# Optimization experiments

Measured on AMD Instinct MI355X. Metric: run time of the kernel, lower is better.

Reference implementation:

```python
import jax, jax.numpy as jnp
import numpy as np

HIDDEN = 1024
HEADS = 16
HEAD_DIM = HIDDEN // HEADS


def setup_inputs() -> dict:
    key = jax.random.key(0)
    k1, k2, k3, k4, k5 = jax.random.split(key, 5)
    B, S = 2, 2048
    x = jax.random.normal(k1, (B, S, HIDDEN), dtype=jnp.float32)
    attention_mask = jnp.ones((B, S), dtype=jnp.int32)
    scale = 1.0 / np.sqrt(HIDDEN)
    W_qkv = jax.random.normal(k2, (HIDDEN, 3 * HIDDEN), dtype=jnp.float32) * scale
    b_qkv = jnp.zeros((3 * HIDDEN,), dtype=jnp.float32)
    W_out = jax.random.normal(k3, (HIDDEN, HIDDEN), dtype=jnp.float32) * scale
    b_out = jnp.zeros((HIDDEN,), dtype=jnp.float32)
    return {"x": x, "attention_mask": attention_mask, "W_qkv": W_qkv,
            "b_qkv": b_qkv, "W_out": W_out, "b_out": b_out}


def reference(x, attention_mask, W_qkv, b_qkv, W_out, b_out):
    B, S, H = x.shape
    qkv = x @ W_qkv + b_qkv                       # [B,S,3H]
    q, k, v = jnp.split(qkv, 3, axis=-1)
    def heads(t):
        return t.reshape(B, S, HEADS, HEAD_DIM).transpose(0, 2, 1, 3)  # [B,h,S,d]
    q, k, v = heads(q), heads(k), heads(v)
    scale = 1.0 / np.sqrt(HEAD_DIM).astype(np.float32)
    scores = jnp.einsum('bhsd,bhtd->bhst', q, k) * scale  # [B,h,S,S]
    causal = jnp.triu(jnp.full((S, S), -jnp.inf, dtype=scores.dtype), k=1)
    scores = scores + causal
    pad = (attention_mask == 0)[:, None, None, :]          # [B,1,1,S]
    scores = jnp.where(pad, -jnp.inf, scores)
    probs = jax.nn.softmax(scores, axis=-1)
    context = jnp.einsum('bhst,bhtd->bhsd', probs, v)
    context = context.transpose(0, 2, 1, 3).reshape(B, S, H)
    output = context @ W_out + b_out
    return (output, q, k, v)
```

## Files before the change

kernel.cpp:

```cpp
#include <hip/hip_runtime.h>
#include <hip/hip_bf16.h>
#include <stdint.h>

typedef __attribute__((ext_vector_type(8))) short bf16x8;
typedef __attribute__((ext_vector_type(4))) float f32x4;

#define GLD16(gp, lp) __builtin_amdgcn_global_load_lds( \
    (const __attribute__((address_space(1))) void*)(gp), \
    (__attribute__((address_space(3))) void*)(lp), 16, 0, 0)

struct bf16_4 { __hip_bfloat16 x, y, z, w; };

__global__ __launch_bounds__(256) void k_conv(const float* __restrict__ in,
                                              __hip_bfloat16* __restrict__ out, int n4)
{
    int i = blockIdx.x * 256 + threadIdx.x;
    if (i >= n4) return;
    float4 v = ((const float4*)in)[i];
    bf16_4 o = { __float2bfloat16(v.x), __float2bfloat16(v.y),
                 __float2bfloat16(v.z), __float2bfloat16(v.w) };
    ((bf16_4*)out)[i] = o;
}

__global__ __launch_bounds__(256) void k_tconv(const float* __restrict__ in,
                                               __hip_bfloat16* __restrict__ out,
                                               int R, int C)
{
    __shared__ float tile[32][33];
    int c0 = blockIdx.x * 32, r0 = blockIdx.y * 32;
    int tc = threadIdx.x & 31, tr = threadIdx.x >> 5;
#pragma unroll
    for (int i = 0; i < 4; i++)
        tile[tr + i * 8][tc] = in[(size_t)(r0 + tr + i * 8) * C + c0 + tc];
    __syncthreads();
#pragma unroll
    for (int i = 0; i < 4; i++) {
        int r = tr + i * 8;
        out[(size_t)(c0 + r) * R + r0 + tc] = __float2bfloat16(tile[tc][r]);
    }
}

__global__ __launch_bounds__(256) void k_vtrans(const __hip_bfloat16* __restrict__ vin,
                                                __hip_bfloat16* __restrict__ vout)
{
    __shared__ __hip_bfloat16 t[64 * 80];
    const int kt = blockIdx.x, bh = blockIdx.y;
    const int tid = threadIdx.x;
    const size_t ib = (size_t)bh * 131072;
#pragma unroll
    for (int i = 0; i < 2; i++) {
        int c = i * 256 + tid;
        int kv = c >> 3, d0 = (c & 7) * 8;
        bf16x8 vv = *(const bf16x8*)(vin + ib + (size_t)(kt * 64 + kv) * 64 + d0);
#pragma unroll
        for (int j = 0; j < 8; j++)
            t[(d0 + j) * 80 + kv] = ((const __hip_bfloat16*)&vv)[j];
    }
    __syncthreads();
#pragma unroll
    for (int i = 0; i < 2; i++) {
        int c = i * 256 + tid;
        int d = c >> 3, kv0 = (c & 7) * 8;
        *(bf16x8*)(vout + ib + (size_t)d * 2048 + kt * 64 + kv0) =
            *(const bf16x8*)(t + d * 80 + kv0);
    }
}

template <int BM, int BN, int TM, int TN, int EPI>
__global__ __launch_bounds__(TM * TN * 64, 2) void k_gemm2(
    const __hip_bfloat16* __restrict__ A,
    const __hip_bfloat16* __restrict__ Bt,
    const float* __restrict__ bias,
    float* __restrict__ outf,
    __hip_bfloat16* __restrict__ outb,
    int M, int N, int K)
{
    constexpr int THREADS = TM * TN * 64;
    constexpr int NMI = BM / TM / 16;
    constexpr int NNI = BN / TN / 16;
    constexpr int ACH = BM * 8 / THREADS;
    constexpr int BCH = BN * 8 / THREADS;

    __shared__ __hip_bfloat16 As[2][BM * 64];
    __shared__ __hip_bfloat16 Bs[2][BN * 64];

    const int tid  = threadIdx.x;
    const int lane = tid & 63, wid = tid >> 6;
    const int wm = wid / TN, wn = wid % TN;
    const int lr = lane & 15, lg = lane >> 4;
    const int m0 = blockIdx.y * BM, n0 = blockIdx.x * BN;
    const int NT = K >> 6;

    f32x4 acc[NMI][NNI] = {};

    auto stage = [&](int bb, int t) {
#pragma unroll
        for (int i = 0; i < ACH; i++) {
            int c = i * THREADS + tid;
            int r = c >> 3, sl = c & 7;
            GLD16(A + (size_t)(m0 + r) * K + t * 64 + ((sl ^ (r & 7)) * 8),
                  &As[bb][(size_t)(i * THREADS + wid * 64) * 8]);
        }
#pragma unroll
        for (int i = 0; i < BCH; i++) {
            int c = i * THREADS + tid;
            int r = c >> 3, sl = c & 7;
            GLD16(Bt + (size_t)(n0 + r) * K + t * 64 + ((sl ^ (r & 7)) * 8),
                  &Bs[bb][(size_t)(i * THREADS + wid * 64) * 8]);
        }
    };

    stage(0, 0);
    __syncthreads();
    int cur = 0;
#pragma unroll 1
    for (int t = 0; t < NT; ++t) {
        if (t + 1 < NT) stage(cur ^ 1, t + 1);
        __builtin_amdgcn_s_setprio(1);
        bf16x8 bfr[NNI][2];
#pragma unroll
        for (int ni = 0; ni < NNI; ni++) {
            int r = wn * (BN / TN) + ni * 16 + lr;
#pragma unroll
            for (int kk = 0; kk < 2; kk++)
                bfr[ni][kk] = *(const bf16x8*)(&Bs[cur][r * 64 + (((kk * 4 + lg) ^ (r & 7)) * 8)]);
        }
#pragma unroll
        for (int mi = 0; mi < NMI; mi++) {
            int r = wm * (BM / TM) + mi * 16 + lr;
            bf16x8 a0 = *(const bf16x8*)(&As[cur][r * 64 + (((0 + lg) ^ (r & 7)) * 8)]);
            bf16x8 a1 = *(const bf16x8*)(&As[cur][r * 64 + (((4 + lg) ^ (r & 7)) * 8)]);
#pragma unroll
            for (int ni = 0; ni < NNI; ni++) {
                acc[mi][ni] = __builtin_amdgcn_mfma_f32_16x16x32_bf16(a0, bfr[ni][0], acc[mi][ni], 0, 0, 0);
                acc[mi][ni] = __builtin_amdgcn_mfma_f32_16x16x32_bf16(a1, bfr[ni][1], acc[mi][ni], 0, 0, 0);
            }
        }
        __builtin_amdgcn_s_setprio(0);
        __syncthreads();
        cur ^= 1;
    }

#pragma unroll
    for (int mi = 0; mi < NMI; mi++) {
#pragma unroll
        for (int ni = 0; ni < NNI; ni++) {
#pragma unroll
            for (int j = 0; j < 4; j++) {
                int mg = m0 + wm * (BM / TM) + mi * 16 + 4 * lg + j;
                int ng = n0 + wn * (BN / TN) + ni * 16 + lr;
                float val = acc[mi][ni][j] + bias[ng];
                if (EPI == 0) {
                    int part = ng >> 10;
                    int h    = (ng >> 6) & 15;
                    int dd   = ng & 63;
                    int b    = mg >> 11;
                    int s    = mg & 2047;
                    size_t idx = ((size_t)part << 22) + ((((size_t)b * 16 + h) * 2048 + s) << 6) + dd;
                    outf[idx] = val;
                    outb[idx] = __float2bfloat16(val);
                } else {
                    outf[(size_t)mg * N + ng] = val;
                }
            }
        }
    }
}

__global__ __launch_bounds__(256, 3) void k_attn2(const __hip_bfloat16* __restrict__ qkv,
                                                  const __hip_bfloat16* __restrict__ vT,
                                                  const int* __restrict__ amask,
                                                  __hip_bfloat16* __restrict__ ctx)
{
    const int bx = blockIdx.x;
    const int bh = blockIdx.y;
    const int b = bh >> 4, h = bh & 15;
    const int tid = threadIdx.x;
    const int lane = tid & 63, w = tid >> 6;
    const int lr = lane & 15, lg = lane >> 4;
    const size_t hb = (size_t)bh * (2048 * 64);
    const __hip_bfloat16* qg = qkv + hb;
    const __hip_bfloat16* kg = qkv + ((size_t)1 << 22) + hb;
    const __hip_bfloat16* vt = vT + (size_t)bh * (64 * 2048);

    __shared__ __hip_bfloat16 Ks[128 * 64];
    __shared__ __hip_bfloat16 Vs[64 * 128];
    __shared__ __hip_bfloat16 Ps[4][16 * 128];
    __shared__ float maskadd[128];

#pragma unroll 1
    for (int pass = 0; pass < 2; ++pass) {
        const int qt = pass ? bx : (31 - bx);
        const int q0 = qt * 64;
        const int nkt = (64 * qt + 191) >> 7;

        bf16x8 qf[2];
#pragma unroll
        for (int kk = 0; kk < 2; kk++)
            qf[kk] = *(const bf16x8*)(qg + (size_t)(q0 + w * 16 + lr) * 64 + kk * 32 + 8 * lg);

        f32x4 of[4] = {};
        float m_run[4], l_run[4];
#pragma unroll
        for (int j = 0; j < 4; j++) { m_run[j] = -1e30f; l_run[j] = 0.f; }
        const int rowg = q0 + w * 16 + 4 * lg;

#pragma unroll 1
        for (int kt = 0; kt < nkt; ++kt) {
            const int k0 = kt * 128;
            __syncthreads();
#pragma unroll
            for (int i = 0; i < 4; i++) {
                int c = i * 256 + tid;
                int r = c >> 3, sl = c & 7;
                GLD16(kg + (size_t)(k0 + r) * 64 + ((sl ^ (r & 7)) * 8),
                      Ks + (size_t)(i * 256 + w * 64) * 8);
            }
#pragma unroll
            for (int i = 0; i < 4; i++) {
                int c = i * 256 + tid;
                int r = c >> 4, sl = c & 15;
                GLD16(vt + (size_t)r * 2048 + k0 + ((sl ^ (r & 15)) * 8),
                      Vs + (size_t)(i * 256 + w * 64) * 8);
            }
            if (tid < 128) maskadd[tid] = amask[b * 2048 + k0 + tid] ? 0.f : -1e30f;
            __syncthreads();

            f32x4 sa[8] = {};
#pragma unroll
            for (int ni = 0; ni < 8; ni++) {
                int r = ni * 16 + lr;
#pragma unroll
                for (int kk = 0; kk < 2; kk++) {
                    bf16x8 kf = *(const bf16x8*)(Ks + (size_t)r * 64 + (((kk * 4 + lg) ^ (r & 7)) * 8));
                    sa[ni] = __builtin_amdgcn_mfma_f32_16x16x32_bf16(qf[kk], kf, sa[ni], 0, 0, 0);
                }
            }
#pragma unroll
            for (int ni = 0; ni < 8; ni++) {
                int colg = k0 + ni * 16 + lr;
                float ma = maskadd[ni * 16 + lr];
#pragma unroll
                for (int j = 0; j < 4; j++) {
                    float val = sa[ni][j] * 0.125f + ma;
                    if (colg > rowg + j) val = -1e30f;
                    sa[ni][j] = val;
                }
            }
            float mnew[4], corr[4];
#pragma unroll
            for (int j = 0; j < 4; j++) {
                float t = fmaxf(fmaxf(fmaxf(sa[0][j], sa[1][j]), fmaxf(sa[2][j], sa[3][j])),
                                fmaxf(fmaxf(sa[4][j], sa[5][j]), fmaxf(sa[6][j], sa[7][j])));
                t = fmaxf(t, __shfl_xor(t, 1));
                t = fmaxf(t, __shfl_xor(t, 2));
                t = fmaxf(t, __shfl_xor(t, 4));
                t = fmaxf(t, __shfl_xor(t, 8));
                mnew[j] = fmaxf(m_run[j], t);
                corr[j] = __expf(m_run[j] - mnew[j]);
                m_run[j] = mnew[j];
            }
            float tsum[4] = {0.f, 0.f, 0.f, 0.f};
#pragma unroll
            for (int ni = 0; ni < 8; ni++)
#pragma unroll
                for (int j = 0; j < 4; j++) {
                    float p = __expf(sa[ni][j] - mnew[j]);
                    sa[ni][j] = p;
                    tsum[j] += p;
                }
#pragma unroll
            for (int j = 0; j < 4; j++) {
                float t = tsum[j];
                t += __shfl_xor(t, 1);
                t += __shfl_xor(t, 2);
                t += __shfl_xor(t, 4);
                t += __shfl_xor(t, 8);
                l_run[j] = l_run[j] * corr[j] + t;
#pragma unroll
                for (int nd = 0; nd < 4; nd++) of[nd][j] *= corr[j];
            }
#pragma unroll
            for (int ni = 0; ni < 8; ni++)
#pragma unroll
                for (int j = 0; j < 4; j++) {
                    int row = 4 * lg + j, col = ni * 16 + lr;
                    Ps[w][row * 128 + (((col >> 3) ^ row) * 8) + (col & 7)] =
                        __float2bfloat16(sa[ni][j]);
                }
            asm volatile("s_waitcnt lgkmcnt(0)" ::: "memory");
            __builtin_amdgcn_sched_barrier(0);
#pragma unroll
            for (int kk = 0; kk < 4; kk++) {
                bf16x8 pf = *(const bf16x8*)(&Ps[w][lr * 128 + (((kk * 4 + lg) ^ lr) * 8)]);
#pragma unroll
                for (int nd = 0; nd < 4; nd++) {
                    int r = nd * 16 + lr;
                    bf16x8 vf = *(const bf16x8*)(Vs + (size_t)r * 128 + (((kk * 4 + lg) ^ (r & 15)) * 8));
                    of[nd] = __builtin_amdgcn_mfma_f32_16x16x32_bf16(pf, vf, of[nd], 0, 0, 0);
                }
            }
        }
#pragma unroll
        for (int j = 0; j < 4; j++) {
            float inv = 1.f / l_run[j];
            int s = rowg + j;
            size_t base = ((size_t)b * 2048 + s) * 1024 + h * 64;
#pragma unroll
            for (int nd = 0; nd < 4; nd++)
                ctx[base + nd * 16 + lr] = __float2bfloat16(of[nd][j] * inv);
        }
    }
}

extern "C" void kernel_launch(void* const* d_in, const int* in_sizes, int n_in,
                              void* d_out, int out_size, void* d_ws, size_t ws_size,
                              hipStream_t stream)
{
    const float* x    = (const float*)d_in[0];
    const int*   am   = (const int*)d_in[1];
    const float* Wqkv = (const float*)d_in[2];
    const float* bqkv = (const float*)d_in[3];
    const float* Wout = (const float*)d_in[4];
    const float* bout = (const float*)d_in[5];
    float* out = (float*)d_out;

    char* ws = (char*)d_ws;
    __hip_bfloat16* x_bf   = (__hip_bfloat16*)(ws);
    __hip_bfloat16* Wqkv_t = (__hip_bfloat16*)(ws + ((size_t)8 << 20));
    __hip_bfloat16* Wout_t = (__hip_bfloat16*)(ws + ((size_t)14 << 20));
    __hip_bfloat16* qkv_bf = (__hip_bfloat16*)(ws + ((size_t)16 << 20));
    __hip_bfloat16* ctx_bf = (__hip_bfloat16*)(ws + ((size_t)40 << 20));
    __hip_bfloat16* vT     = x_bf;

    k_conv<<<4096, 256, 0, stream>>>(x, x_bf, 1048576);
    k_tconv<<<dim3(96, 32), 256, 0, stream>>>(Wqkv, Wqkv_t, 1024, 3072);
    k_tconv<<<dim3(32, 32), 256, 0, stream>>>(Wout, Wout_t, 1024, 1024);
    k_gemm2<256, 192, 2, 4, 0><<<dim3(16, 16), 512, 0, stream>>>(
        x_bf, Wqkv_t, bqkv, out + ((size_t)1 << 22), qkv_bf, 4096, 3072, 1024);
    k_vtrans<<<dim3(32, 32), 256, 0, stream>>>(qkv_bf + ((size_t)2 << 22), vT);
    k_attn2<<<dim3(16, 32), 256, 0, stream>>>(qkv_bf, vT, am, ctx_bf);
    k_gemm2<128, 128, 2, 2, 1><<<dim3(8, 32), 256, 0, stream>>>(
        ctx_bf, Wout_t, bout, out, nullptr, 4096, 1024, 1024);
}
```

Before: 231.6 us.

## Restructure attention to read K/V from global memory, one Q tile per block

The attention kernel stops staging K and V tiles in shared memory and loads MFMA operands directly from global memory (through L2/L1), which removes the block-wide barriers. The two-pass causal load pairing is replaced by one query tile per block on a 32x32 grid with a higher occupancy hint. The mask is loaded per lane, and the causal masking branch is skipped for tiles entirely below the diagonal. Softmax switches to exp2 with the scale folded in by log2(e). Direct global loads are uncoalesced and rely on cache hits, and dropping the pass pairing gives up the causal load balancing.

```diff
diff --git a/kernel.cpp b/kernel.cpp
--- a/kernel.cpp
+++ b/kernel.cpp
@@ -1,6 +1,7 @@
 #include <hip/hip_runtime.h>
 #include <hip/hip_bf16.h>
 #include <stdint.h>
+#include <math.h>
 
 typedef __attribute__((ext_vector_type(8))) short bf16x8;
 typedef __attribute__((ext_vector_type(4))) float f32x4;
@@ -167,149 +168,134 @@
     }
 }
 
-__global__ __launch_bounds__(256, 3) void k_attn2(const __hip_bfloat16* __restrict__ qkv,
+__global__ __launch_bounds__(256, 4) void k_attn3(const __hip_bfloat16* __restrict__ qkv,
                                                   const __hip_bfloat16* __restrict__ vT,
                                                   const int* __restrict__ amask,
                                                   __hip_bfloat16* __restrict__ ctx)
 {
-    const int bx = blockIdx.x;
+    const int qt = 31 - blockIdx.x;
     const int bh = blockIdx.y;
     const int b = bh >> 4, h = bh & 15;
     const int tid = threadIdx.x;
     const int lane = tid & 63, w = tid >> 6;
     const int lr = lane & 15, lg = lane >> 4;
+    const int q0 = qt * 64;
     const size_t hb = (size_t)bh * (2048 * 64);
     const __hip_bfloat16* qg = qkv + hb;
     const __hip_bfloat16* kg = qkv + ((size_t)1 << 22) + hb;
     const __hip_bfloat16* vt = vT + (size_t)bh * (64 * 2048);
 
-    __shared__ __hip_bfloat16 Ks[128 * 64];
-    __shared__ __hip_bfloat16 Vs[64 * 128];
     __shared__ __hip_bfloat16 Ps[4][16 * 128];
-    __shared__ float maskadd[128];
+
+    bf16x8 qf[2];
+#pragma unroll
+    for (int kk = 0; kk < 2; kk++)
+        qf[kk] = *(const bf16x8*)(qg + (size_t)(q0 + w * 16 + lr) * 64 + kk * 32 + 8 * lg);
+
+    f32x4 of[4] = {};
+    float m_run[4], l_run[4];
+#pragma unroll
+    for (int j = 0; j < 4; j++) { m_run[j] = -1e30f; l_run[j] = 0.f; }
+    const int wrow0 = q0 + w * 16;
+    const int rowg = wrow0 + 4 * lg;
+    const int nkt = (q0 + 64 + 127) >> 7;
+    const float SC = 0.18033688011112042f;
 
 #pragma unroll 1
-    for (int pass = 0; pass < 2; ++pass) {
-        const int qt = pass ? bx : (31 - bx);
-        const int q0 = qt * 64;
-        const int nkt = (64 * qt + 191) >> 7;
-
-        bf16x8 qf[2];
-#pragma unroll
-        for (int kk = 0; kk < 2; kk++)
-            qf[kk] = *(const bf16x8*)(qg + (size_t)(q0 + w * 16 + lr) * 64 + kk * 32 + 8 * lg);
-
-        f32x4 of[4] = {};
-        float m_run[4], l_run[4];
-#pragma unroll
-        for (int j = 0; j < 4; j++) { m_run[j] = -1e30f; l_run[j] = 0.f; }
-        const int rowg = q0 + w * 16 + 4 * lg;
-
-#pragma unroll 1
-        for (int kt = 0; kt < nkt; ++kt) {
-            const int k0 = kt * 128;
-            __syncthreads();
-#pragma unroll
-            for (int i = 0; i < 4; i++) {
-                int c = i * 256 + tid;
-                int r = c >> 3, sl = c & 7;
-                GLD16(kg + (size_t)(k0 + r) * 64 + ((sl ^ (r & 7)) * 8),
-                      Ks + (size_t)(i * 256 + w * 64) * 8);
-            }
-#pragma unroll
-            for (int i = 0; i < 4; i++) {
-                int c = i * 256 + tid;
-                int r = c >> 4, sl = c & 15;
-                GLD16(vt + (size_t)r * 2048 + k0 + ((sl ^ (r & 15)) * 8),
-                      Vs + (size_t)(i * 256 + w * 64) * 8);
-            }
-            if (tid < 128) maskadd[tid] = amask[b * 2048 + k0 + tid] ? 0.f : -1e30f;
-            __syncthreads();
-
-            f32x4 sa[8] = {};
-#pragma unroll
-            for (int ni = 0; ni < 8; ni++) {
-                int r = ni * 16 + lr;
-#pragma unroll
-                for (int kk = 0; kk < 2; kk++) {
-                    bf16x8 kf = *(const bf16x8*)(Ks + (size_t)r * 64 + (((kk * 4 + lg) ^ (r & 7)) * 8));
-                    sa[ni] = __builtin_amdgcn_mfma_f32_16x16x32_bf16(qf[kk], kf, sa[ni], 0, 0, 0);
-                }
-            }
+    for (int kt = 0; kt < nkt; ++kt) {
+        const int k0 = kt * 128;
+        float ma[8];
+#pragma unroll
+        for (int ni = 0; ni < 8; ni++)
+            ma[ni] = amask[b * 2048 + k0 + ni * 16 + lr] ? 0.f : -1e30f;
+        f32x4 sa[8] = {};
+#pragma unroll
+        for (int ni = 0; ni < 8; ni++) {
+#pragma unroll
+            for (int kk = 0; kk < 2; kk++) {
+                bf16x8 kf = *(const bf16x8*)(kg + (size_t)(k0 + ni * 16 + lr) * 64 + kk * 32 + 8 * lg);
+                sa[ni] = __builtin_amdgcn_mfma_f32_16x16x32_bf16(qf[kk], kf, sa[ni], 0, 0, 0);
+            }
+        }
+        if (k0 + 127 <= wrow0) {
+#pragma unroll
+            for (int ni = 0; ni < 8; ni++)
+#pragma unroll
+                for (int j = 0; j < 4; j++)
+                    sa[ni][j] = fmaf(sa[ni][j], SC, ma[ni]);
+        } else {
 #pragma unroll
             for (int ni = 0; ni < 8; ni++) {
                 int colg = k0 + ni * 16 + lr;
-                float ma = maskadd[ni * 16 + lr];
 #pragma unroll
                 for (int j = 0; j < 4; j++) {
-                    float val = sa[ni][j] * 0.125f + ma;
+                    float val = fmaf(sa[ni][j], SC, ma[ni]);
                     if (colg > rowg + j) val = -1e30f;
                     sa[ni][j] = val;
                 }
             }
-            float mnew[4], corr[4];
+        }
+        float mnew[4], corr[4];
+#pragma unroll
+        for (int j = 0; j < 4; j++) {
+            float t = fmaxf(fmaxf(fmaxf(sa[0][j], sa[1][j]), fmaxf(sa[2][j], sa[3][j])),
+                            fmaxf(fmaxf(sa[4][j], sa[5][j]), fmaxf(sa[6][j], sa[7][j])));
+            t = fmaxf(t, __shfl_xor(t, 1));
+            t = fmaxf(t, __shfl_xor(t, 2));
+            t = fmaxf(t, __shfl_xor(t, 4));
+            t = fmaxf(t, __shfl_xor(t, 8));
+            mnew[j] = fmaxf(m_run[j], t);
+            corr[j] = exp2f(m_run[j] - mnew[j]);
+            m_run[j] = mnew[j];
+        }
+        float tsum[4] = {0.f, 0.f, 0.f, 0.f};
+#pragma unroll
+        for (int ni = 0; ni < 8; ni++)
 #pragma unroll
             for (int j = 0; j < 4; j++) {
-                float t = fmaxf(fmaxf(fmaxf(sa[0][j], sa[1][j]), fmaxf(sa[2][j], sa[3][j])),
-                                fmaxf(fmaxf(sa[4][j], sa[5][j]), fmaxf(sa[6][j], sa[7][j])));
-                t = fmaxf(t, __shfl_xor(t, 1));
-                t = fmaxf(t, __shfl_xor(t, 2));
-                t = fmaxf(t, __shfl_xor(t, 4));
-                t = fmaxf(t, __shfl_xor(t, 8));
-                mnew[j] = fmaxf(m_run[j], t);
-                corr[j] = __expf(m_run[j] - mnew[j]);
-                m_run[j] = mnew[j];
-            }
-            float tsum[4] = {0.f, 0.f, 0.f, 0.f};
-#pragma unroll
-            for (int ni = 0; ni < 8; ni++)
-#pragma unroll
-                for (int j = 0; j < 4; j++) {
-                    float p = __expf(sa[ni][j] - mnew[j]);
-                    sa[ni][j] = p;
-                    tsum[j] += p;
-                }
+                float p = exp2f(sa[ni][j] - mnew[j]);
+                sa[ni][j] = p;
+                tsum[j] += p;
+            }
+#pragma unroll
+        for (int j = 0; j < 4; j++) {
+            float t = tsum[j];
+            t += __shfl_xor(t, 1);
+            t += __shfl_xor(t, 2);
+            t += __shfl_xor(t, 4);
+            t += __shfl_xor(t, 8);
+            l_run[j] = l_run[j] * corr[j] + t;
+#pragma unroll
+            for (int nd = 0; nd < 4; nd++) of[nd][j] *= corr[j];
+        }
+#pragma unroll
+        for (int ni = 0; ni < 8; ni++)
 #pragma unroll
             for (int j = 0; j < 4; j++) {
-                float t = tsum[j];
-                t += __shfl_xor(t, 1);
-                t += __shfl_xor(t, 2);
-                t += __shfl_xor(t, 4);
-                t += __shfl_xor(t, 8);
-                l_run[j] = l_run[j] * corr[j] + t;
-#pragma unroll
-                for (int nd = 0; nd < 4; nd++) of[nd][j] *= corr[j];
-            }
-#pragma unroll
-            for (int ni = 0; ni < 8; ni++)
-#pragma unroll
-                for (int j = 0; j < 4; j++) {
-                    int row = 4 * lg + j, col = ni * 16 + lr;
-                    Ps[w][row * 128 + (((col >> 3) ^ row) * 8) + (col & 7)] =
-                        __float2bfloat16(sa[ni][j]);
-                }
-            asm volatile("s_waitcnt lgkmcnt(0)" ::: "memory");
-            __builtin_amdgcn_sched_barrier(0);
-#pragma unroll
-            for (int kk = 0; kk < 4; kk++) {
-                bf16x8 pf = *(const bf16x8*)(&Ps[w][lr * 128 + (((kk * 4 + lg) ^ lr) * 8)]);
-#pragma unroll
-                for (int nd = 0; nd < 4; nd++) {
-                    int r = nd * 16 + lr;
-                    bf16x8 vf = *(const bf16x8*)(Vs + (size_t)r * 128 + (((kk * 4 + lg) ^ (r & 15)) * 8));
-                    of[nd] = __builtin_amdgcn_mfma_f32_16x16x32_bf16(pf, vf, of[nd], 0, 0, 0);
-                }
-            }
-        }
-#pragma unroll
-        for (int j = 0; j < 4; j++) {
-            float inv = 1.f / l_run[j];
-            int s = rowg + j;
-            size_t base = ((size_t)b * 2048 + s) * 1024 + h * 64;
-#pragma unroll
-            for (int nd = 0; nd < 4; nd++)
-                ctx[base + nd * 16 + lr] = __float2bfloat16(of[nd][j] * inv);
-        }
+                int row = 4 * lg + j, col = ni * 16 + lr;
+                Ps[w][row * 128 + (((col >> 3) ^ row) * 8) + (col & 7)] =
+                    __float2bfloat16(sa[ni][j]);
+            }
+        asm volatile("s_waitcnt lgkmcnt(0)" ::: "memory");
+        __builtin_amdgcn_sched_barrier(0);
+#pragma unroll
+        for (int kk = 0; kk < 4; kk++) {
+            bf16x8 pf = *(const bf16x8*)(&Ps[w][lr * 128 + (((kk * 4 + lg) ^ lr) * 8)]);
+#pragma unroll
+            for (int nd = 0; nd < 4; nd++) {
+                bf16x8 vf = *(const bf16x8*)(vt + (size_t)(nd * 16 + lr) * 2048 + k0 + kk * 32 + 8 * lg);
+                of[nd] = __builtin_amdgcn_mfma_f32_16x16x32_bf16(pf, vf, of[nd], 0, 0, 0);
+            }
+        }
+    }
+#pragma unroll
+    for (int j = 0; j < 4; j++) {
+        float inv = 1.f / l_run[j];
+        int s = rowg + j;
+        size_t base = ((size_t)b * 2048 + s) * 1024 + h * 64;
+#pragma unroll
+        for (int nd = 0; nd < 4; nd++)
+            ctx[base + nd * 16 + lr] = __float2bfloat16(of[nd][j] * inv);
     }
 }
 
@@ -339,7 +325,7 @@
     k_gemm2<256, 192, 2, 4, 0><<<dim3(16, 16), 512, 0, stream>>>(
         x_bf, Wqkv_t, bqkv, out + ((size_t)1 << 22), qkv_bf, 4096, 3072, 1024);
     k_vtrans<<<dim3(32, 32), 256, 0, stream>>>(qkv_bf + ((size_t)2 << 22), vT);
-    k_attn2<<<dim3(16, 32), 256, 0, stream>>>(qkv_bf, vT, am, ctx_bf);
+    k_attn3<<<dim3(32, 32), 256, 0, stream>>>(qkv_bf, vT, am, ctx_bf);
     k_gemm2<128, 128, 2, 2, 1><<<dim3(8, 32), 256, 0, stream>>>(
         ctx_bf, Wout_t, bout, out, nullptr, 4096, 1024, 1024);
 }
```

New measurement: 534.7 us. 131% more time.

## Register-prefetch next K/V tile in attention, use exp2 softmax and skip mask

Applied to the files above, without the earlier changes.

The attention kernel now loads the next K/V tile into registers while computing the current one, then stores it to LDS at the start of the next iteration. This replaces the direct global-to-LDS loads and is meant to hide global latency. It also folds log2(e) into the score scale so softmax can use exp2f, skips the causal compare on tiles that lie entirely below the diagonal, and raises wave priority around the MFMA blocks. The cost is extra VGPRs for the prefetch buffers, which at launch bounds (256,3) could cause spills or lower occupancy.

```diff
diff --git a/kernel.cpp b/kernel.cpp
--- a/kernel.cpp
+++ b/kernel.cpp
@@ -1,6 +1,7 @@
 #include <hip/hip_runtime.h>
 #include <hip/hip_bf16.h>
 #include <stdint.h>
+#include <math.h>
 
 typedef __attribute__((ext_vector_type(8))) short bf16x8;
 typedef __attribute__((ext_vector_type(4))) float f32x4;
@@ -167,7 +168,7 @@
     }
 }
 
-__global__ __launch_bounds__(256, 3) void k_attn2(const __hip_bfloat16* __restrict__ qkv,
+__global__ __launch_bounds__(256, 3) void k_attn5(const __hip_bfloat16* __restrict__ qkv,
                                                   const __hip_bfloat16* __restrict__ vT,
                                                   const int* __restrict__ amask,
                                                   __hip_bfloat16* __restrict__ ctx)
@@ -188,6 +189,8 @@
     __shared__ __hip_bfloat16 Ps[4][16 * 128];
     __shared__ float maskadd[128];
 
+    const float SC = 0.18033688011112042f;
+
 #pragma unroll 1
     for (int pass = 0; pass < 2; ++pass) {
         const int qt = pass ? bx : (31 - bx);
@@ -203,7 +206,16 @@
         float m_run[4], l_run[4];
 #pragma unroll
         for (int j = 0; j < 4; j++) { m_run[j] = -1e30f; l_run[j] = 0.f; }
-        const int rowg = q0 + w * 16 + 4 * lg;
+        const int wrow0 = q0 + w * 16;
+        const int rowg = wrow0 + 4 * lg;
+
+        bf16x8 kreg[4], vreg[4];
+#pragma unroll
+        for (int i = 0; i < 4; i++) {
+            int c = i * 256 + tid;
+            kreg[i] = *(const bf16x8*)(kg + (size_t)(c >> 3) * 64 + (c & 7) * 8);
+            vreg[i] = *(const bf16x8*)(vt + (size_t)(c >> 4) * 2048 + (c & 15) * 8);
+        }
 
 #pragma unroll 1
         for (int kt = 0; kt < nkt; ++kt) {
@@ -212,20 +224,25 @@
 #pragma unroll
             for (int i = 0; i < 4; i++) {
                 int c = i * 256 + tid;
-                int r = c >> 3, sl = c & 7;
-                GLD16(kg + (size_t)(k0 + r) * 64 + ((sl ^ (r & 7)) * 8),
-                      Ks + (size_t)(i * 256 + w * 64) * 8);
-            }
-#pragma unroll
-            for (int i = 0; i < 4; i++) {
-                int c = i * 256 + tid;
-                int r = c >> 4, sl = c & 15;
-                GLD16(vt + (size_t)r * 2048 + k0 + ((sl ^ (r & 15)) * 8),
-                      Vs + (size_t)(i * 256 + w * 64) * 8);
+                int kr = c >> 3, ksl = c & 7;
+                *(bf16x8*)(Ks + (size_t)kr * 64 + ((ksl ^ (kr & 7)) * 8)) = kreg[i];
+                int vr = c >> 4, vsl = c & 15;
+                *(bf16x8*)(Vs + (size_t)vr * 128 + ((vsl ^ (vr & 15)) * 8)) = vreg[i];
             }
             if (tid < 128) maskadd[tid] = amask[b * 2048 + k0 + tid] ? 0.f : -1e30f;
+            bf16x8 kn[4], vn[4];
+            if (kt + 1 < nkt) {
+                const int k1 = k0 + 128;
+#pragma unroll
+                for (int i = 0; i < 4; i++) {
+                    int c = i * 256 + tid;
+                    kn[i] = *(const bf16x8*)(kg + (size_t)(k1 + (c >> 3)) * 64 + (c & 7) * 8);
+                    vn[i] = *(const bf16x8*)(vt + (size_t)(c >> 4) * 2048 + k1 + (c & 15) * 8);
+                }
+            }
             __syncthreads();
 
+            __builtin_amdgcn_s_setprio(1);
             f32x4 sa[8] = {};
 #pragma unroll
             for (int ni = 0; ni < 8; ni++) {
@@ -236,15 +253,26 @@
                     sa[ni] = __builtin_amdgcn_mfma_f32_16x16x32_bf16(qf[kk], kf, sa[ni], 0, 0, 0);
                 }
             }
-#pragma unroll
-            for (int ni = 0; ni < 8; ni++) {
-                int colg = k0 + ni * 16 + lr;
-                float ma = maskadd[ni * 16 + lr];
-#pragma unroll
-                for (int j = 0; j < 4; j++) {
-                    float val = sa[ni][j] * 0.125f + ma;
-                    if (colg > rowg + j) val = -1e30f;
-                    sa[ni][j] = val;
+            __builtin_amdgcn_s_setprio(0);
+            if (k0 + 127 <= wrow0) {
+#pragma unroll
+                for (int ni = 0; ni < 8; ni++) {
+                    float ma = maskadd[ni * 16 + lr];
+#pragma unroll
+                    for (int j = 0; j < 4; j++)
+                        sa[ni][j] = fmaf(sa[ni][j], SC, ma);
+                }
+            } else {
+#pragma unroll
+                for (int ni = 0; ni < 8; ni++) {
+                    int colg = k0 + ni * 16 + lr;
+                    float ma = maskadd[ni * 16 + lr];
+#pragma unroll
+                    for (int j = 0; j < 4; j++) {
+                        float val = fmaf(sa[ni][j], SC, ma);
+                        if (colg > rowg + j) val = -1e30f;
+                        sa[ni][j] = val;
+                    }
                 }
             }
             float mnew[4], corr[4];
@@ -257,7 +285,7 @@
                 t = fmaxf(t, __shfl_xor(t, 4));
                 t = fmaxf(t, __shfl_xor(t, 8));
                 mnew[j] = fmaxf(m_run[j], t);
-                corr[j] = __expf(m_run[j] - mnew[j]);
+                corr[j] = exp2f(m_run[j] - mnew[j]);
                 m_run[j] = mnew[j];
             }
             float tsum[4] = {0.f, 0.f, 0.f, 0.f};
@@ -265,7 +293,7 @@
             for (int ni = 0; ni < 8; ni++)
 #pragma unroll
                 for (int j = 0; j < 4; j++) {
-                    float p = __expf(sa[ni][j] - mnew[j]);
+                    float p = exp2f(sa[ni][j] - mnew[j]);
                     sa[ni][j] = p;
                     tsum[j] += p;
                 }
@@ -290,6 +318,7 @@
                 }
             asm volatile("s_waitcnt lgkmcnt(0)" ::: "memory");
             __builtin_amdgcn_sched_barrier(0);
+            __builtin_amdgcn_s_setprio(1);
 #pragma unroll
             for (int kk = 0; kk < 4; kk++) {
                 bf16x8 pf = *(const bf16x8*)(&Ps[w][lr * 128 + (((kk * 4 + lg) ^ lr) * 8)]);
@@ -300,6 +329,9 @@
                     of[nd] = __builtin_amdgcn_mfma_f32_16x16x32_bf16(pf, vf, of[nd], 0, 0, 0);
                 }
             }
+            __builtin_amdgcn_s_setprio(0);
+#pragma unroll
+            for (int i = 0; i < 4; i++) { kreg[i] = kn[i]; vreg[i] = vn[i]; }
         }
 #pragma unroll
         for (int j = 0; j < 4; j++) {
@@ -339,7 +371,7 @@
     k_gemm2<256, 192, 2, 4, 0><<<dim3(16, 16), 512, 0, stream>>>(
         x_bf, Wqkv_t, bqkv, out + ((size_t)1 << 22), qkv_bf, 4096, 3072, 1024);
     k_vtrans<<<dim3(32, 32), 256, 0, stream>>>(qkv_bf + ((size_t)2 << 22), vT);
-    k_attn2<<<dim3(16, 32), 256, 0, stream>>>(qkv_bf, vT, am, ctx_bf);
+    k_attn5<<<dim3(16, 32), 256, 0, stream>>>(qkv_bf, vT, am, ctx_bf);
     k_gemm2<128, 128, 2, 2, 1><<<dim3(8, 32), 256, 0, stream>>>(
         ctx_bf, Wout_t, bout, out, nullptr, 4096, 1024, 1024);
 }
```

After: 437.5 us. +88.9%, slower.
